# Kernel optimization log

Hardware: AMD Instinct MI355X
Metric: run time of the kernel (lower is better)

The kernel has to match this reference:

```python
import jax, jax.numpy as jnp
import numpy as np

N = 100000      # nodes (H3 lattice cells)
E = 600000      # directed edges (avg degree ~6, hexagonal)
D_IN, D_H, D_E = 256, 128, 64


def _init_linear(key, fan_in, fan_out):
    kw, kb = jax.random.split(key)
    s = 1.0 / np.sqrt(fan_in)
    W = jax.random.uniform(kw, (fan_in, fan_out), jnp.float32, -s, s)
    b = jax.random.uniform(kb, (fan_out,), jnp.float32, -s, s)
    return W, b


def setup_inputs() -> dict:
    key = jax.random.key(0)
    ks = jax.random.split(key, 8)
    W1, b1 = _init_linear(ks[2], D_IN, D_H)
    W2, b2 = _init_linear(ks[3], D_H, D_H)
    W3, b3 = _init_linear(ks[4], D_H, D_E)
    Wd1, bd1 = _init_linear(ks[5], D_E, D_H)
    Wd2, bd2 = _init_linear(ks[6], D_H, D_IN)
    return {
        "x": jax.random.normal(ks[0], (N, D_IN), jnp.float32),
        "edge_index": jax.random.randint(ks[1], (2, E), 0, N, dtype=jnp.int64),
        "W1": W1, "b1": b1, "W2": W2, "b2": b2, "W3": W3, "b3": b3,
        "Wd1": Wd1, "bd1": bd1, "Wd2": Wd2, "bd2": bd2,
    }


def _gcn_conv(x, src, dst, W, b):
    """PyG GCNConv: add self-loops, sym deg^{-1/2} norm, linear, scatter-add, bias."""
    n = x.shape[0]
    h = x @ W                                                  # [N, out]
    ones = jnp.ones(src.shape[0], x.dtype)
    deg = jax.ops.segment_sum(ones, dst, num_segments=n) + 1.0  # +1 for self-loop
    dinv = jax.lax.rsqrt(deg)                                   # deg >= 1 always
    coef = dinv[src] * dinv[dst]                                # [E]
    agg = jax.ops.segment_sum(h[src] * coef[:, None], dst, num_segments=n)
    agg = agg + h * (dinv * dinv)[:, None]                      # self-loop term
    return agg + b


def reference(x, edge_index, W1, b1, W2, b2, W3, b3, Wd1, bd1, Wd2, bd2):
    src, dst = edge_index[0], edge_index[1]
    # Encoder (dropout is identity in eval mode)
    h = jax.nn.relu(_gcn_conv(x, src, dst, W1, b1))
    h = jax.nn.relu(_gcn_conv(h, src, dst, W2, b2))
    z = _gcn_conv(h, src, dst, W3, b3)                          # [N, D_E]
    # Decoder
    x_hat = jax.nn.relu(z @ Wd1 + bd1) @ Wd2 + bd2              # [N, D_IN]
    return (z, x_hat)
```

## Files before the change

kernel.cpp:

```cpp
#include <hip/hip_runtime.h>

#define DIN 256
#define DH  128
#define DE  64

typedef __attribute__((ext_vector_type(8))) short short8;
typedef __attribute__((ext_vector_type(4))) float f32x4;
typedef __attribute__((ext_vector_type(4))) unsigned short us4;

__device__ inline unsigned short f2bf(float f) {
    unsigned u = __float_as_uint(f);
    return (unsigned short)((u + 0x7FFFu + ((u >> 16) & 1u)) >> 16);
}
__device__ inline float bf2f(unsigned short h) {
    return __uint_as_float((unsigned)h << 16);
}

__device__ inline void gload16(const void* g, void* l) {
    __builtin_amdgcn_global_load_lds(
        (const __attribute__((address_space(1))) void*)g,
        (__attribute__((address_space(3))) void*)l, 16, 0, 0);
}


__global__ void init_counts_kernel(int* __restrict__ counts, int n) {
    int i = blockIdx.x * blockDim.x + threadIdx.x;
    if (i < n) counts[i] = 0;
}

__global__ void count_edges_kernel(const int* __restrict__ dst,
                                   int* __restrict__ counts, int E) {
    int e = blockIdx.x * blockDim.x + threadIdx.x;
    if (e < E) atomicAdd(&counts[dst[e]], 1);
}

__global__ void dinv_kernel(const int* __restrict__ counts,
                            float* __restrict__ dinv, int n) {
    int i = blockIdx.x * blockDim.x + threadIdx.x;
    if (i < n) dinv[i] = rsqrtf((float)counts[i] + 1.0f);
}

__global__ void scan1_kernel(const int* __restrict__ counts,
                             int* __restrict__ rowptr,
                             int* __restrict__ blocksums, int n) {
    __shared__ int sd[256];
    int t = threadIdx.x;
    int base = blockIdx.x * 1024 + t * 4;
    int v[4];
#pragma unroll
    for (int i = 0; i < 4; i++) v[i] = (base + i < n) ? counts[base + i] : 0;
    int tsum = v[0] + v[1] + v[2] + v[3];
    sd[t] = tsum;
    __syncthreads();
    for (int off = 1; off < 256; off <<= 1) {
        int x = (t >= off) ? sd[t - off] : 0;
        __syncthreads();
        sd[t] += x;
        __syncthreads();
    }
    int p = sd[t] - tsum;
#pragma unroll
    for (int i = 0; i < 4; i++) {
        if (base + i < n) rowptr[base + i] = p;
        p += v[i];
    }
    if (t == 255) blocksums[blockIdx.x] = sd[255];
}

__global__ void scan2_kernel(int* __restrict__ blocksums, int nb) {
    if (threadIdx.x == 0 && blockIdx.x == 0) {
        int run = 0;
        for (int i = 0; i < nb; i++) {
            int x = blocksums[i];
            blocksums[i] = run;
            run += x;
        }
    }
}

__global__ void scan3_kernel(int* __restrict__ rowptr, int* __restrict__ cursor,
                             const int* __restrict__ blocksums, int n, int E) {
    int i = blockIdx.x * blockDim.x + threadIdx.x;
    if (i < n) {
        int r = rowptr[i] + blocksums[i >> 10];
        rowptr[i] = r;
        cursor[i] = r;
    }
    if (i == 0) rowptr[n] = E;
}

__global__ void fill_csr_kernel(const int* __restrict__ src,
                                const int* __restrict__ dst,
                                const float* __restrict__ dinv,
                                int* __restrict__ cursor,
                                int* __restrict__ csr_src,
                                float* __restrict__ csr_coef, int E) {
    int e = blockIdx.x * blockDim.x + threadIdx.x;
    if (e >= E) return;
    int s = src[e], d = dst[e];
    int pos = atomicAdd(&cursor[d], 1);
    csr_src[pos] = s;
    csr_coef[pos] = dinv[s] * dinv[d];
}


__global__ void wtile_kernel(const float* __restrict__ W,
                             unsigned short* __restrict__ WtH,
                             unsigned short* __restrict__ WtL, int K, int N,
                             int CF16) {
    int i = blockIdx.x * blockDim.x + threadIdx.x;
    if (i >= K * N) return;
    int k = i / N, n = i % N;
    float v = W[i];
    unsigned short h = f2bf(v);
    unsigned short lo = f2bf(v - bf2f(h));
    int cb = n / CF16, cl = n % CF16;
    int chunk = k >> 6, kk = k & 63;
    int s = kk >> 3, e = kk & 7;
    size_t idx = (size_t)(cb * (K >> 6) + chunk) * (CF16 * 64) + cl * 64 +
                 ((s ^ (cl & 7)) * 8) + e;
    WtH[idx] = h;
    WtL[idx] = lo;
}


template <int K, int CF, bool AFP32, bool BIAS, bool RELU, bool SPLIT>
__global__ __launch_bounds__(256, 2) void mfma_gemm(
    const void* __restrict__ Agh, const void* __restrict__ Agl,
    const unsigned short* __restrict__ WtH,
    const unsigned short* __restrict__ WtL, const float* __restrict__ bias,
    float* __restrict__ C, unsigned short* __restrict__ Oh,
    unsigned short* __restrict__ Ol, int M, int NN) {
    constexpr int CF16 = CF * 16;
    constexpr int CHUNKS = K / 64;
    __shared__ unsigned short Ath[128 * 64];
    __shared__ unsigned short Atl[128 * 64];
    __shared__ unsigned short Bth[CF16 * 64];
    __shared__ unsigned short Btl[CF16 * 64];

    int t = threadIdx.x;
    int wid = t >> 6;
    int l = t & 63;
    int lr = l & 15, lk = l >> 4;
    int row0 = blockIdx.x * 128;
    int col0 = blockIdx.y * CF16;

    f32x4 acc0[CF], acc1[CF];
#pragma unroll
    for (int j = 0; j < CF; j++) {
        acc0[j] = (f32x4){0.f, 0.f, 0.f, 0.f};
        acc1[j] = (f32x4){0.f, 0.f, 0.f, 0.f};
    }

    for (int c = 0; c < CHUNKS; ++c) {
        int k0 = c * 64;
        size_t bbase = (size_t)(blockIdx.y * CHUNKS + c) * (CF16 * 64);
#pragma unroll
        for (int i = 0; i < CF16 / 32; i++) {
            int idx = (i * 256 + t) * 8;
            gload16(WtH + bbase + idx, &Bth[idx]);
            gload16(WtL + bbase + idx, &Btl[idx]);
        }
        if (AFP32) {
            const float* A = (const float*)Agh;
#pragma unroll
            for (int i = 0; i < 4; i++) {
                int row = i * 32 + (t >> 3);
                int gr = row0 + row;
                if (gr >= M) gr = M - 1;
                int ss = (t & 7) ^ (row & 7);
                const float* sp = A + (size_t)gr * K + k0 + ss * 8;
                float4 f0 = *(const float4*)sp;
                float4 f1 = *(const float4*)(sp + 4);
                float fv[8] = {f0.x, f0.y, f0.z, f0.w,
                               f1.x, f1.y, f1.z, f1.w};
                short8 hv, lv;
#pragma unroll
                for (int e = 0; e < 8; e++) {
                    unsigned short h = f2bf(fv[e]);
                    hv[e] = (short)h;
                    lv[e] = (short)f2bf(fv[e] - bf2f(h));
                }
                int li = (i * 256 + t) * 8;
                *(short8*)&Ath[li] = hv;
                *(short8*)&Atl[li] = lv;
            }
        } else {
            const unsigned short* Ah = (const unsigned short*)Agh;
            const unsigned short* Al = (const unsigned short*)Agl;
#pragma unroll
            for (int i = 0; i < 4; i++) {
                int row = i * 32 + (t >> 3);
                int gr = row0 + row;
                if (gr >= M) gr = M - 1;
                int ss = (t & 7) ^ (row & 7);
                size_t go = (size_t)gr * K + k0 + ss * 8;
                gload16(Ah + go, &Ath[(i * 256 + t) * 8]);
                gload16(Al + go, &Atl[(i * 256 + t) * 8]);
            }
        }
        __syncthreads();

#pragma unroll
        for (int ks = 0; ks < 2; ks++) {
            int r0 = wid * 32 + lr;
            int r1 = r0 + 16;
            int s = ks * 4 + lk;
            short8 a0h = *(const short8*)&Ath[r0 * 64 + (s ^ (r0 & 7)) * 8];
            short8 a0l = *(const short8*)&Atl[r0 * 64 + (s ^ (r0 & 7)) * 8];
            short8 a1h = *(const short8*)&Ath[r1 * 64 + (s ^ (r1 & 7)) * 8];
            short8 a1l = *(const short8*)&Atl[r1 * 64 + (s ^ (r1 & 7)) * 8];
#pragma unroll
            for (int j = 0; j < CF; j++) {
                int bo = (j * 16 + lr) * 64 + ((s ^ (lr & 7)) * 8);
                short8 bh = *(const short8*)&Bth[bo];
                short8 bl = *(const short8*)&Btl[bo];
                acc0[j] = __builtin_amdgcn_mfma_f32_16x16x32_bf16(
                    a0h, bh, acc0[j], 0, 0, 0);
                acc0[j] = __builtin_amdgcn_mfma_f32_16x16x32_bf16(
                    a0l, bh, acc0[j], 0, 0, 0);
                acc0[j] = __builtin_amdgcn_mfma_f32_16x16x32_bf16(
                    a0h, bl, acc0[j], 0, 0, 0);
                acc1[j] = __builtin_amdgcn_mfma_f32_16x16x32_bf16(
                    a1h, bh, acc1[j], 0, 0, 0);
                acc1[j] = __builtin_amdgcn_mfma_f32_16x16x32_bf16(
                    a1l, bh, acc1[j], 0, 0, 0);
                acc1[j] = __builtin_amdgcn_mfma_f32_16x16x32_bf16(
                    a1h, bl, acc1[j], 0, 0, 0);
            }
        }
        __syncthreads();
    }

#pragma unroll
    for (int j = 0; j < CF; j++) {
        int col = col0 + j * 16 + lr;
        float bb = BIAS ? bias[col] : 0.f;
#pragma unroll
        for (int e = 0; e < 4; e++) {
            int r = row0 + wid * 32 + lk * 4 + e;
#pragma unroll
            for (int rf = 0; rf < 2; rf++) {
                int rr = r + rf * 16;
                if (rr >= M) continue;
                float v = (rf ? acc1[j][e] : acc0[j][e]) + bb;
                if (RELU) v = fmaxf(v, 0.f);
                if (SPLIT) {
                    unsigned short h = f2bf(v);
                    Oh[(size_t)rr * NN + col] = h;
                    Ol[(size_t)rr * NN + col] = f2bf(v - bf2f(h));
                } else {
                    C[(size_t)rr * NN + col] = v;
                }
            }
        }
    }
}


template <int D, bool RELU, bool WF32>
__global__ __launch_bounds__(256) void agg_kernel(
    const float* __restrict__ h, const float* __restrict__ dinv,
    const int* __restrict__ rowptr, const int* __restrict__ csr_src,
    const float* __restrict__ csr_coef, const float* __restrict__ bias,
    unsigned short* __restrict__ outh, unsigned short* __restrict__ outl,
    float* __restrict__ outf, int n) {
    constexpr int TPN = D / 16;
    constexpr int NPB = 256 / TPN;
    int v = blockIdx.x * NPB + threadIdx.x / TPN;
    int d = threadIdx.x % TPN;
    if (v >= n) return;

    float di = dinv[v];
    float s2 = di * di;
    const float* hv = h + (size_t)v * D + d * 4;
    float4 acc[4];
#pragma unroll
    for (int i = 0; i < 4; i++) {
        float4 sv = *(const float4*)(hv + i * TPN * 4);
        float4 bv = *(const float4*)&bias[(i * TPN + d) * 4];
        acc[i].x = fmaf(sv.x, s2, bv.x);
        acc[i].y = fmaf(sv.y, s2, bv.y);
        acc[i].z = fmaf(sv.z, s2, bv.z);
        acc[i].w = fmaf(sv.w, s2, bv.w);
    }

    int e0 = rowptr[v], e1 = rowptr[v + 1];
    int e = e0;
    for (; e + 2 <= e1; e += 2) {
        int s0 = csr_src[e], s1 = csr_src[e + 1];
        float c0 = csr_coef[e], c1 = csr_coef[e + 1];
        const float* p0 = h + (size_t)s0 * D + d * 4;
        const float* p1 = h + (size_t)s1 * D + d * 4;
        float4 g0[4], g1[4];
#pragma unroll
        for (int i = 0; i < 4; i++) g0[i] = *(const float4*)(p0 + i * TPN * 4);
#pragma unroll
        for (int i = 0; i < 4; i++) g1[i] = *(const float4*)(p1 + i * TPN * 4);
#pragma unroll
        for (int i = 0; i < 4; i++) {
            acc[i].x = fmaf(g0[i].x, c0, acc[i].x);
            acc[i].y = fmaf(g0[i].y, c0, acc[i].y);
            acc[i].z = fmaf(g0[i].z, c0, acc[i].z);
            acc[i].w = fmaf(g0[i].w, c0, acc[i].w);
            acc[i].x = fmaf(g1[i].x, c1, acc[i].x);
            acc[i].y = fmaf(g1[i].y, c1, acc[i].y);
            acc[i].z = fmaf(g1[i].z, c1, acc[i].z);
            acc[i].w = fmaf(g1[i].w, c1, acc[i].w);
        }
    }
    if (e < e1) {
        int s0 = csr_src[e];
        float c0 = csr_coef[e];
        const float* p0 = h + (size_t)s0 * D + d * 4;
#pragma unroll
        for (int i = 0; i < 4; i++) {
            float4 g = *(const float4*)(p0 + i * TPN * 4);
            acc[i].x = fmaf(g.x, c0, acc[i].x);
            acc[i].y = fmaf(g.y, c0, acc[i].y);
            acc[i].z = fmaf(g.z, c0, acc[i].z);
            acc[i].w = fmaf(g.w, c0, acc[i].w);
        }
    }

#pragma unroll
    for (int i = 0; i < 4; i++) {
        if (RELU) {
            acc[i].x = fmaxf(acc[i].x, 0.f);
            acc[i].y = fmaxf(acc[i].y, 0.f);
            acc[i].z = fmaxf(acc[i].z, 0.f);
            acc[i].w = fmaxf(acc[i].w, 0.f);
        }
        size_t o = (size_t)v * D + (i * TPN + d) * 4;
        float av[4] = {acc[i].x, acc[i].y, acc[i].z, acc[i].w};
        us4 hw, lw;
#pragma unroll
        for (int q = 0; q < 4; q++) {
            unsigned short hh = f2bf(av[q]);
            hw[q] = hh;
            lw[q] = f2bf(av[q] - bf2f(hh));
        }
        *(us4*)&outh[o] = hw;
        *(us4*)&outl[o] = lw;
        if (WF32) *(float4*)&outf[o] = acc[i];
    }
}


extern "C" void kernel_launch(void* const* d_in, const int* in_sizes, int n_in,
                              void* d_out, int out_size, void* d_ws,
                              size_t ws_size, hipStream_t stream) {
    const float* x   = (const float*)d_in[0];
    const int*   ei  = (const int*)d_in[1];
    const float* W1  = (const float*)d_in[2];
    const float* b1  = (const float*)d_in[3];
    const float* W2  = (const float*)d_in[4];
    const float* b2  = (const float*)d_in[5];
    const float* W3  = (const float*)d_in[6];
    const float* b3  = (const float*)d_in[7];
    const float* Wd1 = (const float*)d_in[8];
    const float* bd1 = (const float*)d_in[9];
    const float* Wd2 = (const float*)d_in[10];
    const float* bd2 = (const float*)d_in[11];

    const int N = in_sizes[0] / DIN;
    const int E = in_sizes[1] / 2;
    const int* src = ei;
    const int* dst = ei + E;

    char* w = (char*)d_ws;
    auto alloc = [&](size_t bytes) -> char* {
        char* p = w;
        w += (bytes + 255) & ~(size_t)255;
        return p;
    };
    int*   counts    = (int*)alloc((size_t)N * 4);
    float* dinv      = (float*)alloc((size_t)N * 4);
    int*   rowptr    = (int*)alloc((size_t)(N + 1) * 4);
    int*   cursor    = (int*)alloc((size_t)N * 4);
    int*   blocksums = (int*)alloc(4096);
    int*   csr_src   = (int*)alloc((size_t)E * 4);
    float* csr_coef  = (float*)alloc((size_t)E * 4);
    unsigned short* hh = (unsigned short*)alloc((size_t)N * DH * 2);
    unsigned short* hl = (unsigned short*)alloc((size_t)N * DH * 2);
    unsigned short* W1h  = (unsigned short*)alloc(DIN * DH * 2);
    unsigned short* W1l  = (unsigned short*)alloc(DIN * DH * 2);
    unsigned short* W2h  = (unsigned short*)alloc(DH * DH * 2);
    unsigned short* W2l  = (unsigned short*)alloc(DH * DH * 2);
    unsigned short* W3h  = (unsigned short*)alloc(DH * DE * 2);
    unsigned short* W3l  = (unsigned short*)alloc(DH * DE * 2);
    unsigned short* Wd1h = (unsigned short*)alloc(DE * DH * 2);
    unsigned short* Wd1l = (unsigned short*)alloc(DE * DH * 2);
    unsigned short* Wd2h = (unsigned short*)alloc(DH * DIN * 2);
    unsigned short* Wd2l = (unsigned short*)alloc(DH * DIN * 2);

    float* zout = (float*)d_out;
    float* xhat = zout + (size_t)N * DE;
    float* S1   = xhat;
    unsigned short* zh = (unsigned short*)(xhat + (size_t)N * DH);
    unsigned short* zl = zh + (size_t)N * DE;
    unsigned short* rh = hh;
    unsigned short* rl = hl;

    dim3 blk(256);
    int gN = (N + 255) / 256, gE = (E + 255) / 256;

    init_counts_kernel<<<gN, blk, 0, stream>>>(counts, N);
    count_edges_kernel<<<gE, blk, 0, stream>>>(dst, counts, E);
    dinv_kernel<<<gN, blk, 0, stream>>>(counts, dinv, N);
    int nb = (N + 1023) / 1024;
    scan1_kernel<<<nb, blk, 0, stream>>>(counts, rowptr, blocksums, N);
    scan2_kernel<<<1, 64, 0, stream>>>(blocksums, nb);
    scan3_kernel<<<gN, blk, 0, stream>>>(rowptr, cursor, blocksums, N, E);
    fill_csr_kernel<<<gE, blk, 0, stream>>>(src, dst, dinv, cursor, csr_src,
                                            csr_coef, E);

    wtile_kernel<<<(DIN * DH + 255) / 256, blk, 0, stream>>>(W1, W1h, W1l,
                                                             DIN, DH, 128);
    wtile_kernel<<<(DH * DH + 255) / 256, blk, 0, stream>>>(W2, W2h, W2l,
                                                            DH, DH, 128);
    wtile_kernel<<<(DH * DE + 255) / 256, blk, 0, stream>>>(W3, W3h, W3l,
                                                            DH, DE, 64);
    wtile_kernel<<<(DE * DH + 255) / 256, blk, 0, stream>>>(Wd1, Wd1h, Wd1l,
                                                            DE, DH, 128);
    wtile_kernel<<<(DH * DIN + 255) / 256, blk, 0, stream>>>(Wd2, Wd2h, Wd2l,
                                                             DH, DIN, 128);

    int gm = (N + 127) / 128;

    mfma_gemm<DIN, 8, true, false, false, false><<<dim3(gm, 1), blk, 0,
        stream>>>(x, nullptr, W1h, W1l, nullptr, S1, nullptr, nullptr, N, DH);
    agg_kernel<DH, true, false><<<(N + 31) / 32, blk, 0, stream>>>(
        S1, dinv, rowptr, csr_src, csr_coef, b1, hh, hl, nullptr, N);
    mfma_gemm<DH, 8, false, false, false, false><<<dim3(gm, 1), blk, 0,
        stream>>>(hh, hl, W2h, W2l, nullptr, S1, nullptr, nullptr, N, DH);
    agg_kernel<DH, true, false><<<(N + 31) / 32, blk, 0, stream>>>(
        S1, dinv, rowptr, csr_src, csr_coef, b2, hh, hl, nullptr, N);
    mfma_gemm<DH, 4, false, false, false, false><<<dim3(gm, 1), blk, 0,
        stream>>>(hh, hl, W3h, W3l, nullptr, S1, nullptr, nullptr, N, DE);
    agg_kernel<DE, false, true><<<(N + 63) / 64, blk, 0, stream>>>(
        S1, dinv, rowptr, csr_src, csr_coef, b3, zh, zl, zout, N);
    mfma_gemm<DE, 8, false, true, true, true><<<dim3(gm, 1), blk, 0,
        stream>>>(zh, zl, Wd1h, Wd1l, bd1, nullptr, rh, rl, N, DH);
    mfma_gemm<DH, 8, false, true, false, false><<<dim3(gm, 2), blk, 0,
        stream>>>(rh, rl, Wd2h, Wd2l, bd2, xhat, nullptr, nullptr, N, DIN);
}
```

Measured before the change: 600.5 us.

## Prescale GEMM rows by dinv, drop per-edge coefs, use 64-column GEMM tiles

The symmetric normalization is refactored: each GEMM epilogue multiplies its output rows by dinv, so aggregation becomes a plain neighbor sum (self term included) scaled once by dinv[v]. This removes the csr_coef array, its per-edge loads and the per-edge multiplies. The aggregation loop is also unrolled by four with two accumulators for more memory-level parallelism. Separately, the GEMM is fixed to 64-column tiles with higher occupancy (launch bounds 3) and more blocks in the y dimension, which means the A tile is reloaded for each column block.

```diff
diff --git a/kernel.cpp b/kernel.cpp
--- a/kernel.cpp
+++ b/kernel.cpp
@@ -91,59 +91,56 @@
 
 __global__ void fill_csr_kernel(const int* __restrict__ src,
                                 const int* __restrict__ dst,
-                                const float* __restrict__ dinv,
                                 int* __restrict__ cursor,
-                                int* __restrict__ csr_src,
-                                float* __restrict__ csr_coef, int E) {
+                                int* __restrict__ csr_src, int E) {
     int e = blockIdx.x * blockDim.x + threadIdx.x;
     if (e >= E) return;
     int s = src[e], d = dst[e];
     int pos = atomicAdd(&cursor[d], 1);
     csr_src[pos] = s;
-    csr_coef[pos] = dinv[s] * dinv[d];
 }
 
 
 __global__ void wtile_kernel(const float* __restrict__ W,
                              unsigned short* __restrict__ WtH,
-                             unsigned short* __restrict__ WtL, int K, int N,
-                             int CF16) {
+                             unsigned short* __restrict__ WtL, int K, int N) {
     int i = blockIdx.x * blockDim.x + threadIdx.x;
     if (i >= K * N) return;
     int k = i / N, n = i % N;
     float v = W[i];
     unsigned short h = f2bf(v);
     unsigned short lo = f2bf(v - bf2f(h));
-    int cb = n / CF16, cl = n % CF16;
+    int cb = n >> 6, cl = n & 63;
     int chunk = k >> 6, kk = k & 63;
     int s = kk >> 3, e = kk & 7;
-    size_t idx = (size_t)(cb * (K >> 6) + chunk) * (CF16 * 64) + cl * 64 +
+    size_t idx = (size_t)(cb * (K >> 6) + chunk) * (64 * 64) + cl * 64 +
                  ((s ^ (cl & 7)) * 8) + e;
     WtH[idx] = h;
     WtL[idx] = lo;
 }
 
 
-template <int K, int CF, bool AFP32, bool BIAS, bool RELU, bool SPLIT>
-__global__ __launch_bounds__(256, 2) void mfma_gemm(
+template <int K, bool AFP32, bool BIAS, bool RELU, bool SPLIT, bool PRESCALE>
+__global__ __launch_bounds__(256, 3) void mfma_gemm(
     const void* __restrict__ Agh, const void* __restrict__ Agl,
     const unsigned short* __restrict__ WtH,
     const unsigned short* __restrict__ WtL, const float* __restrict__ bias,
-    float* __restrict__ C, unsigned short* __restrict__ Oh,
-    unsigned short* __restrict__ Ol, int M, int NN) {
-    constexpr int CF16 = CF * 16;
+    const float* __restrict__ dinv, float* __restrict__ C,
+    unsigned short* __restrict__ Oh, unsigned short* __restrict__ Ol, int M,
+    int NN) {
+    constexpr int CF = 4;
     constexpr int CHUNKS = K / 64;
     __shared__ unsigned short Ath[128 * 64];
     __shared__ unsigned short Atl[128 * 64];
-    __shared__ unsigned short Bth[CF16 * 64];
-    __shared__ unsigned short Btl[CF16 * 64];
+    __shared__ unsigned short Bth[64 * 64];
+    __shared__ unsigned short Btl[64 * 64];
 
     int t = threadIdx.x;
     int wid = t >> 6;
     int l = t & 63;
     int lr = l & 15, lk = l >> 4;
     int row0 = blockIdx.x * 128;
-    int col0 = blockIdx.y * CF16;
+    int col0 = blockIdx.y * 64;
 
     f32x4 acc0[CF], acc1[CF];
 #pragma unroll
@@ -154,9 +151,9 @@
 
     for (int c = 0; c < CHUNKS; ++c) {
         int k0 = c * 64;
-        size_t bbase = (size_t)(blockIdx.y * CHUNKS + c) * (CF16 * 64);
-#pragma unroll
-        for (int i = 0; i < CF16 / 32; i++) {
+        size_t bbase = (size_t)(blockIdx.y * CHUNKS + c) * (64 * 64);
+#pragma unroll
+        for (int i = 0; i < 2; i++) {
             int idx = (i * 256 + t) * 8;
             gload16(WtH + bbase + idx, &Bth[idx]);
             gload16(WtL + bbase + idx, &Btl[idx]);
@@ -244,6 +241,7 @@
                 int rr = r + rf * 16;
                 if (rr >= M) continue;
                 float v = (rf ? acc1[j][e] : acc0[j][e]) + bb;
+                if (PRESCALE) v *= dinv[rr];
                 if (RELU) v = fmaxf(v, 0.f);
                 if (SPLIT) {
                     unsigned short h = f2bf(v);
@@ -260,38 +258,58 @@
 
 template <int D, bool RELU, bool WF32>
 __global__ __launch_bounds__(256) void agg_kernel(
-    const float* __restrict__ h, const float* __restrict__ dinv,
+    const float* __restrict__ g, const float* __restrict__ dinv,
     const int* __restrict__ rowptr, const int* __restrict__ csr_src,
-    const float* __restrict__ csr_coef, const float* __restrict__ bias,
-    unsigned short* __restrict__ outh, unsigned short* __restrict__ outl,
-    float* __restrict__ outf, int n) {
+    const float* __restrict__ bias, unsigned short* __restrict__ outh,
+    unsigned short* __restrict__ outl, float* __restrict__ outf, int n) {
     constexpr int TPN = D / 16;
     constexpr int NPB = 256 / TPN;
     int v = blockIdx.x * NPB + threadIdx.x / TPN;
     int d = threadIdx.x % TPN;
     if (v >= n) return;
 
-    float di = dinv[v];
-    float s2 = di * di;
-    const float* hv = h + (size_t)v * D + d * 4;
-    float4 acc[4];
+    const float* gv = g + (size_t)v * D + d * 4;
+    float4 accA[4], accB[4];
 #pragma unroll
     for (int i = 0; i < 4; i++) {
-        float4 sv = *(const float4*)(hv + i * TPN * 4);
-        float4 bv = *(const float4*)&bias[(i * TPN + d) * 4];
-        acc[i].x = fmaf(sv.x, s2, bv.x);
-        acc[i].y = fmaf(sv.y, s2, bv.y);
-        acc[i].z = fmaf(sv.z, s2, bv.z);
-        acc[i].w = fmaf(sv.w, s2, bv.w);
+        accA[i] = *(const float4*)(gv + i * TPN * 4);
+        accB[i] = make_float4(0.f, 0.f, 0.f, 0.f);
     }
 
     int e0 = rowptr[v], e1 = rowptr[v + 1];
     int e = e0;
+    for (; e + 4 <= e1; e += 4) {
+        int s0 = csr_src[e], s1 = csr_src[e + 1];
+        int s2 = csr_src[e + 2], s3 = csr_src[e + 3];
+        const float* p0 = g + (size_t)s0 * D + d * 4;
+        const float* p1 = g + (size_t)s1 * D + d * 4;
+        const float* p2 = g + (size_t)s2 * D + d * 4;
+        const float* p3 = g + (size_t)s3 * D + d * 4;
+        float4 g0[4], g1[4], g2[4], g3[4];
+#pragma unroll
+        for (int i = 0; i < 4; i++) g0[i] = *(const float4*)(p0 + i * TPN * 4);
+#pragma unroll
+        for (int i = 0; i < 4; i++) g1[i] = *(const float4*)(p1 + i * TPN * 4);
+#pragma unroll
+        for (int i = 0; i < 4; i++) g2[i] = *(const float4*)(p2 + i * TPN * 4);
+#pragma unroll
+        for (int i = 0; i < 4; i++) g3[i] = *(const float4*)(p3 + i * TPN * 4);
+#pragma unroll
+        for (int i = 0; i < 4; i++) {
+            accA[i].x += g0[i].x + g2[i].x;
+            accA[i].y += g0[i].y + g2[i].y;
+            accA[i].z += g0[i].z + g2[i].z;
+            accA[i].w += g0[i].w + g2[i].w;
+            accB[i].x += g1[i].x + g3[i].x;
+            accB[i].y += g1[i].y + g3[i].y;
+            accB[i].z += g1[i].z + g3[i].z;
+            accB[i].w += g1[i].w + g3[i].w;
+        }
+    }
     for (; e + 2 <= e1; e += 2) {
         int s0 = csr_src[e], s1 = csr_src[e + 1];
-        float c0 = csr_coef[e], c1 = csr_coef[e + 1];
-        const float* p0 = h + (size_t)s0 * D + d * 4;
-        const float* p1 = h + (size_t)s1 * D + d * 4;
+        const float* p0 = g + (size_t)s0 * D + d * 4;
+        const float* p1 = g + (size_t)s1 * D + d * 4;
         float4 g0[4], g1[4];
 #pragma unroll
         for (int i = 0; i < 4; i++) g0[i] = *(const float4*)(p0 + i * TPN * 4);
@@ -299,40 +317,46 @@
         for (int i = 0; i < 4; i++) g1[i] = *(const float4*)(p1 + i * TPN * 4);
 #pragma unroll
         for (int i = 0; i < 4; i++) {
-            acc[i].x = fmaf(g0[i].x, c0, acc[i].x);
-            acc[i].y = fmaf(g0[i].y, c0, acc[i].y);
-            acc[i].z = fmaf(g0[i].z, c0, acc[i].z);
-            acc[i].w = fmaf(g0[i].w, c0, acc[i].w);
-            acc[i].x = fmaf(g1[i].x, c1, acc[i].x);
-            acc[i].y = fmaf(g1[i].y, c1, acc[i].y);
-            acc[i].z = fmaf(g1[i].z, c1, acc[i].z);
-            acc[i].w = fmaf(g1[i].w, c1, acc[i].w);
+            accA[i].x += g0[i].x;
+            accA[i].y += g0[i].y;
+            accA[i].z += g0[i].z;
+            accA[i].w += g0[i].w;
+            accB[i].x += g1[i].x;
+            accB[i].y += g1[i].y;
+            accB[i].z += g1[i].z;
+            accB[i].w += g1[i].w;
         }
     }
     if (e < e1) {
         int s0 = csr_src[e];
-        float c0 = csr_coef[e];
-        const float* p0 = h + (size_t)s0 * D + d * 4;
+        const float* p0 = g + (size_t)s0 * D + d * 4;
 #pragma unroll
         for (int i = 0; i < 4; i++) {
-            float4 g = *(const float4*)(p0 + i * TPN * 4);
-            acc[i].x = fmaf(g.x, c0, acc[i].x);
-            acc[i].y = fmaf(g.y, c0, acc[i].y);
-            acc[i].z = fmaf(g.z, c0, acc[i].z);
-            acc[i].w = fmaf(g.w, c0, acc[i].w);
-        }
-    }
-
+            float4 gg = *(const float4*)(p0 + i * TPN * 4);
+            accA[i].x += gg.x;
+            accA[i].y += gg.y;
+            accA[i].z += gg.z;
+            accA[i].w += gg.w;
+        }
+    }
+
+    float dv = dinv[v];
 #pragma unroll
     for (int i = 0; i < 4; i++) {
+        float4 bv = *(const float4*)&bias[(i * TPN + d) * 4];
+        float4 r;
+        r.x = fmaf(dv, accA[i].x + accB[i].x, bv.x);
+        r.y = fmaf(dv, accA[i].y + accB[i].y, bv.y);
+        r.z = fmaf(dv, accA[i].z + accB[i].z, bv.z);
+        r.w = fmaf(dv, accA[i].w + accB[i].w, bv.w);
         if (RELU) {
-            acc[i].x = fmaxf(acc[i].x, 0.f);
-            acc[i].y = fmaxf(acc[i].y, 0.f);
-            acc[i].z = fmaxf(acc[i].z, 0.f);
-            acc[i].w = fmaxf(acc[i].w, 0.f);
+            r.x = fmaxf(r.x, 0.f);
+            r.y = fmaxf(r.y, 0.f);
+            r.z = fmaxf(r.z, 0.f);
+            r.w = fmaxf(r.w, 0.f);
         }
         size_t o = (size_t)v * D + (i * TPN + d) * 4;
-        float av[4] = {acc[i].x, acc[i].y, acc[i].z, acc[i].w};
+        float av[4] = {r.x, r.y, r.z, r.w};
         us4 hw, lw;
 #pragma unroll
         for (int q = 0; q < 4; q++) {
@@ -342,7 +366,7 @@
         }
         *(us4*)&outh[o] = hw;
         *(us4*)&outl[o] = lw;
-        if (WF32) *(float4*)&outf[o] = acc[i];
+        if (WF32) *(float4*)&outf[o] = r;
     }
 }
 
@@ -380,7 +404,6 @@
     int*   cursor    = (int*)alloc((size_t)N * 4);
     int*   blocksums = (int*)alloc(4096);
     int*   csr_src   = (int*)alloc((size_t)E * 4);
-    float* csr_coef  = (float*)alloc((size_t)E * 4);
     unsigned short* hh = (unsigned short*)alloc((size_t)N * DH * 2);
     unsigned short* hl = (unsigned short*)alloc((size_t)N * DH * 2);
     unsigned short* W1h  = (unsigned short*)alloc(DIN * DH * 2);
@@ -412,36 +435,39 @@
     scan1_kernel<<<nb, blk, 0, stream>>>(counts, rowptr, blocksums, N);
     scan2_kernel<<<1, 64, 0, stream>>>(blocksums, nb);
     scan3_kernel<<<gN, blk, 0, stream>>>(rowptr, cursor, blocksums, N, E);
-    fill_csr_kernel<<<gE, blk, 0, stream>>>(src, dst, dinv, cursor, csr_src,
-                                            csr_coef, E);
+    fill_csr_kernel<<<gE, blk, 0, stream>>>(src, dst, cursor, csr_src, E);
 
     wtile_kernel<<<(DIN * DH + 255) / 256, blk, 0, stream>>>(W1, W1h, W1l,
-                                                             DIN, DH, 128);
+                                                             DIN, DH);
     wtile_kernel<<<(DH * DH + 255) / 256, blk, 0, stream>>>(W2, W2h, W2l,
-                                                            DH, DH, 128);
+                                                            DH, DH);
     wtile_kernel<<<(DH * DE + 255) / 256, blk, 0, stream>>>(W3, W3h, W3l,
-                                                            DH, DE, 64);
+                                                            DH, DE);
     wtile_kernel<<<(DE * DH + 255) / 256, blk, 0, stream>>>(Wd1, Wd1h, Wd1l,
-                                                            DE, DH, 128);
+                                                            DE, DH);
     wtile_kernel<<<(DH * DIN + 255) / 256, blk, 0, stream>>>(Wd2, Wd2h, Wd2l,
-                                                             DH, DIN, 128);
+                                                             DH, DIN);
 
     int gm = (N + 127) / 128;
 
-    mfma_gemm<DIN, 8, true, false, false, false><<<dim3(gm, 1), blk, 0,
-        stream>>>(x, nullptr, W1h, W1l, nullptr, S1, nullptr, nullptr, N, DH);
+    mfma_gemm<DIN, true, false, false, false, true><<<dim3(gm, 2), blk, 0,
+        stream>>>(x, nullptr, W1h, W1l, nullptr, dinv, S1, nullptr, nullptr,
+                  N, DH);
     agg_kernel<DH, true, false><<<(N + 31) / 32, blk, 0, stream>>>(
-        S1, dinv, rowptr, csr_src, csr_coef, b1, hh, hl, nullptr, N);
-    mfma_gemm<DH, 8, false, false, false, false><<<dim3(gm, 1), blk, 0,
-        stream>>>(hh, hl, W2h, W2l, nullptr, S1, nullptr, nullptr, N, DH);
+        S1, dinv, rowptr, csr_src, b1, hh, hl, nullptr, N);
+    mfma_gemm<DH, false, false, false, false, true><<<dim3(gm, 2), blk, 0,
+        stream>>>(hh, hl, W2h, W2l, nullptr, dinv, S1, nullptr, nullptr,
+                  N, DH);
     agg_kernel<DH, true, false><<<(N + 31) / 32, blk, 0, stream>>>(
-        S1, dinv, rowptr, csr_src, csr_coef, b2, hh, hl, nullptr, N);
-    mfma_gemm<DH, 4, false, false, false, false><<<dim3(gm, 1), blk, 0,
-        stream>>>(hh, hl, W3h, W3l, nullptr, S1, nullptr, nullptr, N, DE);
+        S1, dinv, rowptr, csr_src, b2, hh, hl, nullptr, N);
+    mfma_gemm<DH, false, false, false, false, true><<<dim3(gm, 1), blk, 0,
+        stream>>>(hh, hl, W3h, W3l, nullptr, dinv, S1, nullptr, nullptr,
+                  N, DE);
     agg_kernel<DE, false, true><<<(N + 63) / 64, blk, 0, stream>>>(
-        S1, dinv, rowptr, csr_src, csr_coef, b3, zh, zl, zout, N);
-    mfma_gemm<DE, 8, false, true, true, true><<<dim3(gm, 1), blk, 0,
-        stream>>>(zh, zl, Wd1h, Wd1l, bd1, nullptr, rh, rl, N, DH);
-    mfma_gemm<DH, 8, false, true, false, false><<<dim3(gm, 2), blk, 0,
-        stream>>>(rh, rl, Wd2h, Wd2l, bd2, xhat, nullptr, nullptr, N, DIN);
-}
+        S1, dinv, rowptr, csr_src, b3, zh, zl, zout, N);
+    mfma_gemm<DE, false, true, true, true, false><<<dim3(gm, 2), blk, 0,
+        stream>>>(zh, zl, Wd1h, Wd1l, bd1, nullptr, nullptr, rh, rl, N, DH);
+    mfma_gemm<DH, false, true, false, false, false><<<dim3(gm, 4), blk, 0,
+        stream>>>(rh, rl, Wd2h, Wd2l, bd2, nullptr, xhat, nullptr, nullptr,
+                  N, DIN);
+}
```

New measurement: 628.0 us. 4.6% more time.
